# Kernel tuning notes

Measured on AMD Instinct MI355X. Metric: run time of the kernel, lower is better.

Reference implementation:

```python
import jax, jax.numpy as jnp
import numpy as np

EMBED_DIM = 64
N_EMBED = 1024
BATCH, H, W = 16, 64, 64


def setup_inputs() -> dict:
    key = jax.random.key(0)
    k1, k2 = jax.random.split(key)
    inputs = jax.random.normal(k1, (BATCH, H, W, EMBED_DIM), dtype=jnp.float32)
    # codebook as in Quantize.build: RandomNormal(stddev=1.0), shape (embed_dim, n_embed)
    cluster_mean = jax.random.normal(k2, (EMBED_DIM, N_EMBED), dtype=jnp.float32)
    return {"inputs": inputs, "cluster_mean": cluster_mean}


def reference(inputs, cluster_mean):
    # inputs: [B,H,W,D]; cluster_mean: [D,K]
    D = cluster_mean.shape[0]
    samples = inputs.reshape(-1, D)  # [N,D]
    dist = (
        jnp.sum(samples * samples, axis=1, keepdims=True)
        - 2.0 * (samples @ cluster_mean)
        + jnp.sum(cluster_mean * cluster_mean, axis=0, keepdims=True)
    )
    cluster_index = jnp.argmin(dist, axis=1).reshape(inputs.shape[:-1])  # [B,H,W]
    quantize = cluster_mean.T[cluster_index]  # gather -> [B,H,W,D]
    q_loss = jnp.mean((quantize - jax.lax.stop_gradient(inputs)) ** 2)
    e_loss = jnp.mean((jax.lax.stop_gradient(quantize) - inputs) ** 2)
    loss = q_loss + 0.25 * e_loss
    # straight-through estimator
    outputs = inputs + jax.lax.stop_gradient(quantize - inputs)
    return outputs, cluster_index, loss
```

## Files before the change

kernel.cpp:

```cpp
#include <hip/hip_runtime.h>
#include <stdint.h>

#define NS 65536
#define D 64
#define K 1024
#define NEL 4194304
#define MARGIN_KEY 0.025f

typedef short bf16x8 __attribute__((ext_vector_type(8)));
typedef short s16x4 __attribute__((ext_vector_type(4)));
typedef float f32x4 __attribute__((ext_vector_type(4)));

static __device__ __forceinline__ unsigned short bf16_rne(float x) {
    union { float f; uint32_t u; } v; v.f = x;
    uint32_t r = v.u + 0x7FFFu + ((v.u >> 16) & 1u);
    return (unsigned short)(r >> 16);
}
static __device__ __forceinline__ float bf16f(unsigned short h) {
    union { uint32_t u; float f; } v; v.u = ((uint32_t)h) << 16;
    return v.f;
}

__global__ __launch_bounds__(256) void vq_prep(
    const float* __restrict__ cm,
    unsigned short* __restrict__ P,
    float* __restrict__ cnorm,
    double* __restrict__ acc)
{
    const int tx = threadIdx.x;
    const int col = tx & 15;
    const int dg = tx >> 4;
    const int b = blockIdx.x;
    const int k = b * 16 + col;
    if (b == 0 && tx == 0) *acc = 0.0;

    float p = 0.f;
    s16x4 hv, lv;
#pragma unroll
    for (int j = 0; j < 4; ++j) {
        float v = cm[(dg * 4 + j) * K + k];
        unsigned short hb = bf16_rne(v);
        hv[j] = (short)hb;
        lv[j] = (short)bf16_rne(v - bf16f(hb));
        p = fmaf(v, v, p);
    }
    const int lane = ((dg >> 1) & 3) * 16 + col;
    const int e0 = (dg & 1) * 4;
    unsigned short* ph = P + ((size_t)(b * 4 + (dg >> 3)) * 64 + lane) * 8 + e0;
    unsigned short* pl = P + ((size_t)(b * 4 + 2 + (dg >> 3)) * 64 + lane) * 8 + e0;
    *(s16x4*)ph = hv;
    *(s16x4*)pl = lv;

    __shared__ float pn[16][17];
    pn[col][dg] = p;
    __syncthreads();
    if (tx < 16) {
        float s = 0.f;
#pragma unroll
        for (int g = 0; g < 16; ++g) s += pn[tx][g];
        cnorm[b * 16 + tx] = s;
    }
}

__global__ __launch_bounds__(256, 2) void vq_main(
    const float* __restrict__ xin,
    const float* __restrict__ cm,
    const unsigned short* __restrict__ P,
    const float* __restrict__ cnorm,
    float* __restrict__ outq,
    float* __restrict__ outidx,
    double* __restrict__ acc_g)
{
    __shared__ char smemA[36864];
    __shared__ float cn_lds[1024];
    __shared__ int   widx[128];

    unsigned short* xh = (unsigned short*)smemA;
    unsigned short* xl = (unsigned short*)(smemA + 18432);
    float* mb1 = (float*)smemA;
    float* mb2 = (float*)(smemA + 8704);
    int*   mi1 = (int*)(smemA + 17408);
    int*   mi2 = (int*)(smemA + 26112);
    float* red = (float*)smemA;

    const int tx = threadIdx.x;
    const int S0 = blockIdx.x * 128;
    const int w = tx >> 6, l = tx & 63;
    const int quad = l >> 4, col = l & 15;

    const unsigned short* pb = P + (size_t)l * 8;

#define LDB(B0, B1, B2, B3, T) do {                                   \
        const unsigned short* q_ = pb + (size_t)(T) * 2048;           \
        B0 = *(const bf16x8*)(q_);                                    \
        B1 = *(const bf16x8*)(q_ + 512);                              \
        B2 = *(const bf16x8*)(q_ + 1024);                             \
        B3 = *(const bf16x8*)(q_ + 1536);                             \
    } while (0)

    bf16x8 c0, c1, c2, c3, n0, n1, n2, n3;
    LDB(c0, c1, c2, c3, 0);
    LDB(n0, n1, n2, n3, 1);

    {
        const int s = tx >> 2, d0 = (tx & 3) * 16;
#pragma unroll
        for (int half = 0; half < 2; ++half) {
            const int ss = s + half * 64;
            const float* gp = xin + (size_t)(S0 + ss) * D + d0;
            bf16x8 hv0, hv1, lv0, lv1;
#pragma unroll
            for (int j = 0; j < 8; ++j) {
                float va = -gp[j], vb = -gp[8 + j];
                unsigned short ha = bf16_rne(va), hb = bf16_rne(vb);
                hv0[j] = (short)ha; hv1[j] = (short)hb;
                lv0[j] = (short)bf16_rne(va - bf16f(ha));
                lv1[j] = (short)bf16_rne(vb - bf16f(hb));
            }
            *(bf16x8*)(xh + ss * 72 + d0)     = hv0;
            *(bf16x8*)(xh + ss * 72 + d0 + 8) = hv1;
            *(bf16x8*)(xl + ss * 72 + d0)     = lv0;
            *(bf16x8*)(xl + ss * 72 + d0 + 8) = lv1;
        }
#pragma unroll
        for (int q = 0; q < 4; ++q)
            cn_lds[q * 256 + tx] = 0.5f * cnorm[q * 256 + tx];
    }
    __syncthreads();

    bf16x8 AH0[2], AH1[2], AL0[2], AL1[2];
#pragma unroll
    for (int sg = 0; sg < 2; ++sg) {
        const int srow = w * 32 + sg * 16 + col;
        AH0[sg] = *(const bf16x8*)(xh + srow * 72 + quad * 8);
        AH1[sg] = *(const bf16x8*)(xh + srow * 72 + 32 + quad * 8);
        AL0[sg] = *(const bf16x8*)(xl + srow * 72 + quad * 8);
        AL1[sg] = *(const bf16x8*)(xl + srow * 72 + 32 + quad * 8);
    }

    float b1[2][4], b2[2][4]; int i1[2][4], i2[2][4];
#pragma unroll
    for (int sg = 0; sg < 2; ++sg)
#pragma unroll
        for (int r = 0; r < 4; ++r) {
            b1[sg][r] = 3.4e38f; b2[sg][r] = 3.4e38f;
            i1[sg][r] = 0; i2[sg][r] = 0;
        }

#define COMPUTE(B0, B1, B2, B3, T) do {                                        \
        const int kc_ = (T) * 16 + col;                                        \
        const float cv_ = cn_lds[kc_];                                         \
        const f32x4 cc_ = {cv_, cv_, cv_, cv_};                                \
        _Pragma("unroll")                                                      \
        for (int sg = 0; sg < 2; ++sg) {                                       \
            f32x4 a_ = cc_;                                                    \
            a_ = __builtin_amdgcn_mfma_f32_16x16x32_bf16(AH0[sg], B0, a_, 0, 0, 0); \
            a_ = __builtin_amdgcn_mfma_f32_16x16x32_bf16(AH1[sg], B1, a_, 0, 0, 0); \
            a_ = __builtin_amdgcn_mfma_f32_16x16x32_bf16(AH0[sg], B2, a_, 0, 0, 0); \
            a_ = __builtin_amdgcn_mfma_f32_16x16x32_bf16(AH1[sg], B3, a_, 0, 0, 0); \
            a_ = __builtin_amdgcn_mfma_f32_16x16x32_bf16(AL0[sg], B0, a_, 0, 0, 0); \
            a_ = __builtin_amdgcn_mfma_f32_16x16x32_bf16(AL1[sg], B1, a_, 0, 0, 0); \
            _Pragma("unroll")                                                  \
            for (int r = 0; r < 4; ++r) {                                      \
                float v_ = a_[r];                                              \
                bool c1_ = v_ < b1[sg][r];                                     \
                bool c2_ = v_ < b2[sg][r];                                     \
                b2[sg][r] = __builtin_amdgcn_fmed3f(b1[sg][r], v_, b2[sg][r]); \
                b1[sg][r] = fminf(b1[sg][r], v_);                              \
                i2[sg][r] = c1_ ? i1[sg][r] : (c2_ ? kc_ : i2[sg][r]);         \
                i1[sg][r] = c1_ ? kc_ : i1[sg][r];                             \
            }                                                                  \
        }                                                                      \
    } while (0)

    for (int t = 0; t < 64; t += 2) {
        COMPUTE(c0, c1, c2, c3, t);
        if (t + 2 < 64) LDB(c0, c1, c2, c3, t + 2);
        COMPUTE(n0, n1, n2, n3, t + 1);
        if (t + 3 < 64) LDB(n0, n1, n2, n3, t + 3);
    }

    __syncthreads();
#pragma unroll
    for (int sg = 0; sg < 2; ++sg) {
        const int u = (w * 2 + sg) * 64 + l;
        const int sk = 4 * (u + (u >> 4));
#pragma unroll
        for (int r = 0; r < 4; ++r) {
            mb1[sk + r] = b1[sg][r];
            mb2[sk + r] = b2[sg][r];
            mi1[sk + r] = i1[sg][r];
            mi2[sk + r] = i2[sg][r];
        }
    }
    __syncthreads();

    if (tx < 128) {
        const int mw = tx >> 5, msg = (tx >> 4) & 1, mq = (tx >> 2) & 3, mr = tx & 3;
        float B1 = 3.4e38f, B2 = 3.4e38f; int I1 = 0, I2 = 0;
#pragma unroll
        for (int c = 0; c < 16; ++c) {
            const int u = (mw * 2 + msg) * 64 + mq * 16 + c;
            const int e = 4 * (u + (u >> 4)) + mr;
            float v1 = mb1[e]; int j1 = mi1[e];
            float v2 = mb2[e]; int j2 = mi2[e];
            if (v1 < B1)      { B2 = B1; I2 = I1; B1 = v1; I1 = j1; }
            else if (v1 < B2) { B2 = v1; I2 = j1; }
            if (v2 < B1)      { B2 = B1; I2 = I1; B1 = v2; I1 = j2; }
            else if (v2 < B2) { B2 = v2; I2 = j2; }
        }
        int winner = I1;
        if (B2 - B1 < MARGIN_KEY) {
            const float* xp = xin + (size_t)(S0 + tx) * D;
            float a0 = 0, a1 = 0, a2 = 0, a3 = 0, e0 = 0, e1 = 0, e2 = 0, e3 = 0;
            for (int dd = 0; dd < D; dd += 4) {
                float x0 = xp[dd], x1 = xp[dd + 1], x2 = xp[dd + 2], x3 = xp[dd + 3];
                a0 = fmaf(x0, cm[(dd + 0) * K + I1], a0);
                a1 = fmaf(x1, cm[(dd + 1) * K + I1], a1);
                a2 = fmaf(x2, cm[(dd + 2) * K + I1], a2);
                a3 = fmaf(x3, cm[(dd + 3) * K + I1], a3);
                e0 = fmaf(x0, cm[(dd + 0) * K + I2], e0);
                e1 = fmaf(x1, cm[(dd + 1) * K + I2], e1);
                e2 = fmaf(x2, cm[(dd + 2) * K + I2], e2);
                e3 = fmaf(x3, cm[(dd + 3) * K + I2], e3);
            }
            float d1 = cn_lds[I1] - ((a0 + a1) + (a2 + a3));
            float d2 = cn_lds[I2] - ((e0 + e1) + (e2 + e3));
            if (d2 < d1 || (d2 == d1 && I2 < I1)) winner = I2;
        }
        widx[tx] = winner;
    }
    __syncthreads();

    float psum = 0.f;
#pragma unroll
    for (int half = 0; half < 2; ++half) {
        const int sl = (tx >> 2) + half * 64, d0 = (tx & 3) * 16;
        const int gs = S0 + sl;
        const int wi = widx[sl];
        const int gt = wi >> 4, gc = wi & 15;
        const int qq = (d0 >> 3) & 3;
        const int gf = d0 >> 5;
        const unsigned short* gh = P + ((size_t)((gt * 4 + gf) * 64) + qq * 16 + gc) * 8;
        const unsigned short* gl = P + ((size_t)((gt * 4 + 2 + gf) * 64) + qq * 16 + gc) * 8;
        bf16x8 h0 = *(const bf16x8*)(gh);
        bf16x8 h1 = *(const bf16x8*)(gh + 128);
        bf16x8 l0 = *(const bf16x8*)(gl);
        bf16x8 l1 = *(const bf16x8*)(gl + 128);
        const float* xr = xin + (size_t)gs * D + d0;
        float* oq = outq + (size_t)gs * D + d0;
#pragma unroll
        for (int g = 0; g < 4; ++g) {
            float4 xv = *(const float4*)(xr + 4 * g);
            float q0 = bf16f((unsigned short)(g < 2 ? h0[4 * g + 0] : h1[4 * g - 8 + 0])) +
                       bf16f((unsigned short)(g < 2 ? l0[4 * g + 0] : l1[4 * g - 8 + 0]));
            float q1 = bf16f((unsigned short)(g < 2 ? h0[4 * g + 1] : h1[4 * g - 8 + 1])) +
                       bf16f((unsigned short)(g < 2 ? l0[4 * g + 1] : l1[4 * g - 8 + 1]));
            float q2 = bf16f((unsigned short)(g < 2 ? h0[4 * g + 2] : h1[4 * g - 8 + 2])) +
                       bf16f((unsigned short)(g < 2 ? l0[4 * g + 2] : l1[4 * g - 8 + 2]));
            float q3 = bf16f((unsigned short)(g < 2 ? h0[4 * g + 3] : h1[4 * g - 8 + 3])) +
                       bf16f((unsigned short)(g < 2 ? l0[4 * g + 3] : l1[4 * g - 8 + 3]));
            float dx = q0 - xv.x, dy = q1 - xv.y, dz = q2 - xv.z, dw = q3 - xv.w;
            float4 o;
            o.x = xv.x + dx; o.y = xv.y + dy; o.z = xv.z + dz; o.w = xv.w + dw;
            *(float4*)(oq + 4 * g) = o;
            psum = fmaf(dx, dx, psum);
            psum = fmaf(dy, dy, psum);
            psum = fmaf(dz, dz, psum);
            psum = fmaf(dw, dw, psum);
        }
    }

    if (tx < 128)
        outidx[S0 + tx] = (float)widx[tx];

    __syncthreads();
    red[tx] = psum;
    __syncthreads();
    for (int st = 128; st > 0; st >>= 1) {
        if (tx < st) red[tx] += red[tx + st];
        __syncthreads();
    }
    if (tx == 0) atomicAdd(acc_g, (double)red[0]);
#undef LDB
#undef COMPUTE
}

__global__ void vq_finalize(const double* __restrict__ acc,
                            float* __restrict__ loss_out)
{
    float m = (float)(*acc / (double)NEL);
    *loss_out = m + 0.25f * m;
}

extern "C" void kernel_launch(void* const* d_in, const int* in_sizes, int n_in,
                              void* d_out, int out_size, void* d_ws, size_t ws_size,
                              hipStream_t stream) {
    const float* xin = (const float*)d_in[0];
    const float* cm  = (const float*)d_in[1];

    float* out     = (float*)d_out;
    float* outq    = out;
    float* outidx  = out + NEL;
    float* outloss = out + NEL + NS;

    unsigned short* P = (unsigned short*)d_ws;
    float*  cnorm = (float*)((char*)d_ws + 262144);
    double* acc   = (double*)((char*)d_ws + 266240);

    vq_prep<<<64, 256, 0, stream>>>(cm, P, cnorm, acc);
    vq_main<<<512, 256, 0, stream>>>(xin, cm, P, cnorm, outq, outidx, acc);
    vq_finalize<<<1, 1, 0, stream>>>(acc, outloss);
}
```

Baseline: 125.0 us.

## Stage codebook tiles via async global-to-LDS loads and pack indices into distance bits

```diff
diff --git a/kernel.cpp b/kernel.cpp
--- a/kernel.cpp
+++ b/kernel.cpp
@@ -72,6 +72,7 @@
     double* __restrict__ acc_g)
 {
     __shared__ char smemA[36864];
+    __shared__ unsigned short btile[4][2048];
     __shared__ float cn_lds[1024];
     __shared__ int   widx[128];
 
@@ -79,8 +80,6 @@
     unsigned short* xl = (unsigned short*)(smemA + 18432);
     float* mb1 = (float*)smemA;
     float* mb2 = (float*)(smemA + 8704);
-    int*   mi1 = (int*)(smemA + 17408);
-    int*   mi2 = (int*)(smemA + 26112);
     float* red = (float*)smemA;
 
     const int tx = threadIdx.x;
@@ -88,19 +87,13 @@
     const int w = tx >> 6, l = tx & 63;
     const int quad = l >> 4, col = l & 15;
 
-    const unsigned short* pb = P + (size_t)l * 8;
-
-#define LDB(B0, B1, B2, B3, T) do {                                   \
-        const unsigned short* q_ = pb + (size_t)(T) * 2048;           \
-        B0 = *(const bf16x8*)(q_);                                    \
-        B1 = *(const bf16x8*)(q_ + 512);                              \
-        B2 = *(const bf16x8*)(q_ + 1024);                             \
-        B3 = *(const bf16x8*)(q_ + 1536);                             \
+#define ISSUE(T) do {                                                          \
+        const unsigned short* g_ = P + (size_t)(T) * 2048 + tx * 8;            \
+        __builtin_amdgcn_global_load_lds(g_, &btile[(T) & 3][tx * 8], 16, 0, 0); \
     } while (0)
-
-    bf16x8 c0, c1, c2, c3, n0, n1, n2, n3;
-    LDB(c0, c1, c2, c3, 0);
-    LDB(n0, n1, n2, n3, 1);
+#define WAITV(N) asm volatile("s_waitcnt vmcnt(" #N ")" ::: "memory")
+
+    ISSUE(0); ISSUE(1); ISSUE(2);
 
     {
         const int s = tx >> 2, d0 = (tx & 3) * 16;
@@ -138,49 +131,51 @@
         AL1[sg] = *(const bf16x8*)(xl + srow * 72 + 32 + quad * 8);
     }
 
-    float b1[2][4], b2[2][4]; int i1[2][4], i2[2][4];
+    float b1[2][4], b2[2][4];
 #pragma unroll
     for (int sg = 0; sg < 2; ++sg)
 #pragma unroll
-        for (int r = 0; r < 4; ++r) {
-            b1[sg][r] = 3.4e38f; b2[sg][r] = 3.4e38f;
-            i1[sg][r] = 0; i2[sg][r] = 0;
-        }
-
-#define COMPUTE(B0, B1, B2, B3, T) do {                                        \
-        const int kc_ = (T) * 16 + col;                                        \
-        const float cv_ = cn_lds[kc_];                                         \
-        const f32x4 cc_ = {cv_, cv_, cv_, cv_};                                \
+        for (int r = 0; r < 4; ++r) { b1[sg][r] = 3.4e38f; b2[sg][r] = 3.4e38f; }
+
+#define BODY(T) do {                                                           \
+        const unsigned short* bt_ = &btile[(T) & 3][0];                        \
+        bf16x8 bh0 = *(const bf16x8*)(bt_ + l * 8);                            \
+        bf16x8 bh1 = *(const bf16x8*)(bt_ + 512 + l * 8);                      \
+        bf16x8 bl0 = *(const bf16x8*)(bt_ + 1024 + l * 8);                     \
+        bf16x8 bl1 = *(const bf16x8*)(bt_ + 1536 + l * 8);                     \
+        const float cnv_ = cn_lds[(T) * 16 + col];                             \
+        const f32x4 cA_ = {cnv_, cnv_, cnv_, cnv_};                            \
+        const f32x4 z4_ = {0.f, 0.f, 0.f, 0.f};                                \
+        const unsigned tt_ = (unsigned)(T);                                    \
         _Pragma("unroll")                                                      \
         for (int sg = 0; sg < 2; ++sg) {                                       \
-            f32x4 a_ = cc_;                                                    \
-            a_ = __builtin_amdgcn_mfma_f32_16x16x32_bf16(AH0[sg], B0, a_, 0, 0, 0); \
-            a_ = __builtin_amdgcn_mfma_f32_16x16x32_bf16(AH1[sg], B1, a_, 0, 0, 0); \
-            a_ = __builtin_amdgcn_mfma_f32_16x16x32_bf16(AH0[sg], B2, a_, 0, 0, 0); \
-            a_ = __builtin_amdgcn_mfma_f32_16x16x32_bf16(AH1[sg], B3, a_, 0, 0, 0); \
-            a_ = __builtin_amdgcn_mfma_f32_16x16x32_bf16(AL0[sg], B0, a_, 0, 0, 0); \
-            a_ = __builtin_amdgcn_mfma_f32_16x16x32_bf16(AL1[sg], B1, a_, 0, 0, 0); \
+            f32x4 a1_ = __builtin_amdgcn_mfma_f32_16x16x32_bf16(AH0[sg], bh0, cA_, 0, 0, 0); \
+            a1_ = __builtin_amdgcn_mfma_f32_16x16x32_bf16(AH1[sg], bh1, a1_, 0, 0, 0); \
+            a1_ = __builtin_amdgcn_mfma_f32_16x16x32_bf16(AL0[sg], bh0, a1_, 0, 0, 0); \
+            f32x4 a2_ = __builtin_amdgcn_mfma_f32_16x16x32_bf16(AH0[sg], bl0, z4_, 0, 0, 0); \
+            a2_ = __builtin_amdgcn_mfma_f32_16x16x32_bf16(AH1[sg], bl1, a2_, 0, 0, 0); \
+            a2_ = __builtin_amdgcn_mfma_f32_16x16x32_bf16(AL1[sg], bh1, a2_, 0, 0, 0); \
             _Pragma("unroll")                                                  \
             for (int r = 0; r < 4; ++r) {                                      \
-                float v_ = a_[r];                                              \
-                bool c1_ = v_ < b1[sg][r];                                     \
-                bool c2_ = v_ < b2[sg][r];                                     \
-                b2[sg][r] = __builtin_amdgcn_fmed3f(b1[sg][r], v_, b2[sg][r]); \
-                b1[sg][r] = fminf(b1[sg][r], v_);                              \
-                i2[sg][r] = c1_ ? i1[sg][r] : (c2_ ? kc_ : i2[sg][r]);         \
-                i1[sg][r] = c1_ ? kc_ : i1[sg][r];                             \
+                float v_ = a1_[r] + a2_[r];                                    \
+                unsigned pu_ = (__builtin_bit_cast(unsigned, v_) & 0xFFFFFFC0u) | tt_; \
+                float f_ = __builtin_bit_cast(float, pu_);                     \
+                b2[sg][r] = __builtin_amdgcn_fmed3f(b1[sg][r], f_, b2[sg][r]); \
+                b1[sg][r] = fminf(b1[sg][r], f_);                              \
             }                                                                  \
         }                                                                      \
     } while (0)
 
-    for (int t = 0; t < 64; t += 2) {
-        COMPUTE(c0, c1, c2, c3, t);
-        if (t + 2 < 64) LDB(c0, c1, c2, c3, t + 2);
-        COMPUTE(n0, n1, n2, n3, t + 1);
-        if (t + 3 < 64) LDB(n0, n1, n2, n3, t + 3);
-    }
-
-    __syncthreads();
+    for (int t = 0; t < 61; ++t) {
+        WAITV(2);
+        __builtin_amdgcn_s_barrier();
+        ISSUE(t + 3);
+        BODY(t);
+    }
+    WAITV(2); __builtin_amdgcn_s_barrier(); BODY(61);
+    WAITV(1); __builtin_amdgcn_s_barrier(); BODY(62);
+    WAITV(0); __builtin_amdgcn_s_barrier(); BODY(63);
+
 #pragma unroll
     for (int sg = 0; sg < 2; ++sg) {
         const int u = (w * 2 + sg) * 64 + l;
@@ -189,8 +184,6 @@
         for (int r = 0; r < 4; ++r) {
             mb1[sk + r] = b1[sg][r];
             mb2[sk + r] = b2[sg][r];
-            mi1[sk + r] = i1[sg][r];
-            mi2[sk + r] = i2[sg][r];
         }
     }
     __syncthreads();
@@ -202,8 +195,10 @@
         for (int c = 0; c < 16; ++c) {
             const int u = (mw * 2 + msg) * 64 + mq * 16 + c;
             const int e = 4 * (u + (u >> 4)) + mr;
-            float v1 = mb1[e]; int j1 = mi1[e];
-            float v2 = mb2[e]; int j2 = mi2[e];
+            float v1 = mb1[e];
+            float v2 = mb2[e];
+            int j1 = (int)(__builtin_bit_cast(unsigned, v1) & 63u) * 16 + c;
+            int j2 = (int)(__builtin_bit_cast(unsigned, v2) & 63u) * 16 + c;
             if (v1 < B1)      { B2 = B1; I2 = I1; B1 = v1; I1 = j1; }
             else if (v1 < B2) { B2 = v1; I2 = j1; }
             if (v2 < B1)      { B2 = B1; I2 = I1; B1 = v2; I1 = j2; }
@@ -282,8 +277,9 @@
         __syncthreads();
     }
     if (tx == 0) atomicAdd(acc_g, (double)red[0]);
-#undef LDB
-#undef COMPUTE
+#undef ISSUE
+#undef WAITV
+#undef BODY
 }
 
 __global__ void vq_finalize(const double* __restrict__ acc,
```

New measurement: 123.1 us. Within noise of the previous version (-1.5%).
